# Performance work log

Measured on AMD Instinct MI355X. Metric: run time of the kernel, lower is better.

## Reference

```python
import jax, jax.numpy as jnp
import numpy as np

N, E, G = 50000, 500000, 1024
ND, ED, H, L, OUT = 32, 16, 128, 4, 1
BN_EPS = 1e-5


def setup_inputs() -> dict:
    key = jax.random.key(0)
    ks = jax.random.split(key, 32)

    def w(k, shape, fan):
        return jax.random.normal(k, shape, jnp.float32) / np.float32(np.sqrt(fan))

    inp = {
        "x": jax.random.normal(ks[0], (N, ND), jnp.float32),
        "edge_index": jax.random.randint(ks[1], (2, E), 0, N, jnp.int64),
        "edge_attr": jax.random.normal(ks[2], (E, ED), jnp.float32),
        "batch": jax.random.randint(ks[3], (N,), 0, G, jnp.int64),
        # embeddings
        "ne_w": w(ks[4], (ND, H), ND), "ne_b": jnp.zeros((H,), jnp.float32),
        "ee_w": w(ks[5], (ED, H), ED), "ee_b": jnp.zeros((H,), jnp.float32),
        # per-layer node_mlp: Linear(2H,H) ReLU Linear(H,H) BN(H)
        "nm_w1": w(ks[6], (L, 2 * H, H), 2 * H), "nm_b1": jnp.zeros((L, H), jnp.float32),
        "nm_w2": w(ks[7], (L, H, H), H), "nm_b2": jnp.zeros((L, H), jnp.float32),
        "bn_g": jnp.ones((L, H), jnp.float32), "bn_b": jnp.zeros((L, H), jnp.float32),
        # per-layer edge_mlp: Linear(H,H) ReLU Linear(H,H)  (edge_dim==hidden_dim inside MPNN)
        "em_w1": w(ks[8], (L, H, H), H), "em_b1": jnp.zeros((L, H), jnp.float32),
        "em_w2": w(ks[9], (L, H, H), H), "em_b2": jnp.zeros((L, H), jnp.float32),
        # readout: Linear(H,H) ReLU Dropout(eval=identity) Linear(H,OUT)
        "ro_w1": w(ks[10], (H, H), H), "ro_b1": jnp.zeros((H,), jnp.float32),
        "ro_w2": w(ks[11], (H, OUT), H), "ro_b2": jnp.zeros((OUT,), jnp.float32),
    }
    return inp


def reference(x, edge_index, edge_attr, batch,
              ne_w, ne_b, ee_w, ee_b,
              nm_w1, nm_b1, nm_w2, nm_b2, bn_g, bn_b,
              em_w1, em_b1, em_w2, em_b2,
              ro_w1, ro_b1, ro_w2, ro_b2):
    src, dst = edge_index[0], edge_index[1]  # PyG default: x_j from source, aggregate at target
    h = x @ ne_w + ne_b                      # [N, H]
    e = edge_attr @ ee_w + ee_b              # [E, H]
    inv_std = np.float32(1.0 / np.sqrt(1.0 + BN_EPS))  # eval BN, running_mean=0, running_var=1
    for l in range(nm_w1.shape[0]):
        # edge_mlp
        e = jax.nn.relu(e @ em_w1[l] + em_b1[l]) @ em_w2[l] + em_b2[l]
        # message: concat(x_j, edge_attr) -> node_mlp
        msg = jnp.concatenate([h[src], e], axis=1)              # [E, 2H]
        msg = jax.nn.relu(msg @ nm_w1[l] + nm_b1[l]) @ nm_w2[l] + nm_b2[l]
        msg = msg * (inv_std * bn_g[l]) + bn_b[l]               # BatchNorm1d (eval)
        # scatter-add aggregation + residual update
        agg = jax.ops.segment_sum(msg, dst, num_segments=h.shape[0])
        h = agg + h
    pooled = jax.ops.segment_sum(h, batch, num_segments=G)      # global_add_pool -> [G, H]
    return jax.nn.relu(pooled @ ro_w1 + ro_b1) @ ro_w2 + ro_b2  # [G, OUT]
```

## Files before the change

kernel.cpp:

```cpp
#include <hip/hip_runtime.h>
#include <hip/hip_bf16.h>
#include <math.h>

#define NN 50000
#define EE 500000
#define GG 1024
#define NDIM 32
#define EDIM 16
#define HH 128
#define LL 4
#define TE 64
#define NTE ((EE + TE - 1) / TE)
#define NB2 ((NN + 127) / 128)
#define SCAN_NB ((NN + 255) / 256)

typedef unsigned short ushortT;
typedef __attribute__((ext_vector_type(8))) short bf16x8;
typedef __attribute__((ext_vector_type(4))) float f32x4;

#define MFMA16(a, b, c) __builtin_amdgcn_mfma_f32_16x16x32_bf16(a, b, c, 0, 0, 0)

__device__ inline float bf2f(ushortT u) {
    union { unsigned int i; float f; } v; v.i = ((unsigned int)u) << 16; return v.f;
}
__device__ inline ushortT f2bf(float f) {
    __hip_bfloat16 h = __float2bfloat16(f);
    return *reinterpret_cast<ushortT*>(&h);
}
__device__ inline short f2bfs(float f) { return (short)f2bf(f); }

__device__ inline bf16x8 lds_a(const char* base, int strideB, int row, int colByte,
                               int mask) {
    int b = row * strideB + colByte;
    b ^= ((row & mask) << 4);
    return *reinterpret_cast<const bf16x8*>(base + b);
}

__global__ __launch_bounds__(256) void hist_kernel(
        const int* __restrict__ dst, int* __restrict__ counts) {
    int i = blockIdx.x * 256 + threadIdx.x;
    if (i < EE) atomicAdd(&counts[dst[i]], 1);
}

__global__ __launch_bounds__(256) void scan_part1(
        const int* __restrict__ counts, int* __restrict__ bsum) {
    __shared__ int buf[256];
    int t = threadIdx.x;
    int i = blockIdx.x * 256 + t;
    buf[t] = (i < NN) ? counts[i] : 0;
    __syncthreads();
    for (int s = 128; s > 0; s >>= 1) {
        if (t < s) buf[t] += buf[t + s];
        __syncthreads();
    }
    if (t == 0) bsum[blockIdx.x] = buf[0];
}

__global__ __launch_bounds__(256) void scan_part2(
        const int* __restrict__ bsum, int* __restrict__ bbase) {
    __shared__ int buf[256];
    int t = threadIdx.x;
    int v = (t < SCAN_NB) ? bsum[t] : 0;
    buf[t] = v;
    __syncthreads();
    for (int off = 1; off < 256; off <<= 1) {
        int s = (t >= off) ? buf[t - off] : 0;
        __syncthreads();
        buf[t] += s;
        __syncthreads();
    }
    if (t < SCAN_NB) bbase[t] = buf[t] - v;
}

__global__ __launch_bounds__(256) void scan_part3(
        const int* __restrict__ counts, const int* __restrict__ bbase,
        int* __restrict__ base) {
    __shared__ int buf[256];
    int t = threadIdx.x;
    int i = blockIdx.x * 256 + t;
    int v = (i < NN) ? counts[i] : 0;
    buf[t] = v;
    __syncthreads();
    for (int off = 1; off < 256; off <<= 1) {
        int s = (t >= off) ? buf[t - off] : 0;
        __syncthreads();
        buf[t] += s;
        __syncthreads();
    }
    if (i < NN) base[i] = bbase[blockIdx.x] + buf[t] - v;
}

__global__ __launch_bounds__(256) void build_perm_kernel(
        const int* __restrict__ src, const int* __restrict__ dst,
        const int* __restrict__ base, int* __restrict__ cnt,
        int* __restrict__ perm, int* __restrict__ srcS, int* __restrict__ dstS) {
    int i = blockIdx.x * 256 + threadIdx.x;
    if (i >= EE) return;
    int d = dst[i];
    int pos = base[d] + atomicAdd(&cnt[d], 1);
    perm[pos] = i;
    srcS[pos] = src[i];
    dstS[pos] = d;
}

__global__ __launch_bounds__(256) void ghist_kernel(
        const int* __restrict__ batch, int* __restrict__ gcounts) {
    int i = blockIdx.x * 256 + threadIdx.x;
    if (i < NN) atomicAdd(&gcounts[batch[i]], 1);
}

__global__ __launch_bounds__(1024) void gscan_kernel(
        const int* __restrict__ gcounts, int* __restrict__ gbase) {
    __shared__ int buf[1024];
    int t = threadIdx.x;
    int v = gcounts[t];
    buf[t] = v;
    __syncthreads();
    for (int off = 1; off < 1024; off <<= 1) {
        int s = (t >= off) ? buf[t - off] : 0;
        __syncthreads();
        buf[t] += s;
        __syncthreads();
    }
    gbase[t] = buf[t] - v;
}

__global__ __launch_bounds__(256) void gbuild_kernel(
        const int* __restrict__ batch, const int* __restrict__ gbase,
        int* __restrict__ gcnt, int* __restrict__ gperm) {
    int i = blockIdx.x * 256 + threadIdx.x;
    if (i >= NN) return;
    int b = batch[i];
    int pos = gbase[b] + atomicAdd(&gcnt[b], 1);
    gperm[pos] = i;
}

__global__ __launch_bounds__(256) void transpose_kernel(
        const float* __restrict__ in, ushortT* __restrict__ out, int K, int N) {
    int per = K * N;
    int total = LL * per;
    int idx = blockIdx.x * 256 + threadIdx.x;
    if (idx >= total) return;
    int l = idx / per, rem = idx - l * per;
    int n = rem / K, k = rem - n * K;
    out[idx] = f2bf(in[(size_t)l * per + (size_t)k * N + n]);
}

__global__ __launch_bounds__(256) void transpose_pad32_kernel(
        const float* __restrict__ in, ushortT* __restrict__ out, int KIN) {
    int idx = blockIdx.x * 256 + threadIdx.x;
    if (idx >= HH * 32) return;
    int n = idx >> 5, k = idx & 31;
    out[idx] = (k < KIN) ? f2bf(in[k * HH + n]) : (ushortT)0;
}

__global__ __launch_bounds__(256) void bnfold_kernel(
        const float* __restrict__ w2, const float* __restrict__ b2,
        const float* __restrict__ bng, const float* __restrict__ bnb,
        ushortT* __restrict__ w2g, float* __restrict__ nb2g, float inv_std) {
    int idx = blockIdx.x * 256 + threadIdx.x;
    if (idx < LL * HH * HH) {
        int l = idx / (HH * HH), rem = idx - l * (HH * HH);
        int n = rem / HH, k = rem - n * HH;
        w2g[idx] = f2bf(w2[(size_t)l * HH * HH + (size_t)k * HH + n] *
                        bng[l * HH + n] * inv_std);
    }
    if (idx < LL * HH) {
        nb2g[idx] = b2[idx] * bng[idx] * inv_std + bnb[idx];
    }
}

template<int K, int KS, bool HASB>
__device__ inline void gemm_b(const char* aBase, int aStrideB, int aMask,
        const ushortT* __restrict__ wT, const float* __restrict__ bias,
        int wr, int wc, int l15, int lg, f32x4 acc[2][4]) {
#pragma unroll
    for (int ntl = 0; ntl < 4; ++ntl) {
        float bb = HASB ? bias[wc * 64 + ntl * 16 + l15] : 0.f;
        f32x4 iv = {bb, bb, bb, bb};
        acc[0][ntl] = iv;
        acc[1][ntl] = iv;
    }
#pragma unroll
    for (int ks = 0; ks < K / 32; ++ks) {
        int kk = ks * 32 + lg * 8;
        bf16x8 a0 = lds_a(aBase, aStrideB, wr * 32 + l15,      kk * 2, aMask);
        bf16x8 a1 = lds_a(aBase, aStrideB, wr * 32 + 16 + l15, kk * 2, aMask);
#pragma unroll
        for (int ntl = 0; ntl < 4; ++ntl) {
            int n = wc * 64 + ntl * 16 + l15;
            bf16x8 b = *reinterpret_cast<const bf16x8*>(wT + (size_t)n * KS + kk);
            acc[0][ntl] = MFMA16(a0, b, acc[0][ntl]);
            acc[1][ntl] = MFMA16(a1, b, acc[1][ntl]);
        }
    }
}

__device__ inline void gemm_uinit3(const char* aBase, const char* uBase,
        const ushortT* __restrict__ wT,
        int wr, int wc, int l15, int lg, f32x4 acc[2][4]) {
#pragma unroll
    for (int mt = 0; mt < 2; ++mt)
#pragma unroll
        for (int ntl = 0; ntl < 4; ++ntl) {
            int col = wc * 64 + ntl * 16 + l15;
#pragma unroll
            for (int r = 0; r < 4; ++r) {
                int row = wr * 32 + mt * 16 + lg * 4 + r;
                int b = row * 256 + col * 2; b ^= ((row & 7) << 4);
                acc[mt][ntl][r] = bf2f(*reinterpret_cast<const ushortT*>(uBase + b));
            }
        }
#pragma unroll
    for (int ks = 0; ks < 4; ++ks) {
        int kk = ks * 32 + lg * 8;
        bf16x8 a0 = lds_a(aBase, 256, wr * 32 + l15,      kk * 2, 7);
        bf16x8 a1 = lds_a(aBase, 256, wr * 32 + 16 + l15, kk * 2, 7);
#pragma unroll
        for (int ntl = 0; ntl < 4; ++ntl) {
            int n = wc * 64 + ntl * 16 + l15;
            bf16x8 b = *reinterpret_cast<const bf16x8*>(wT + (size_t)n * 256 + kk);
            acc[0][ntl] = MFMA16(a0, b, acc[0][ntl]);
            acc[1][ntl] = MFMA16(a1, b, acc[1][ntl]);
        }
    }
}

__device__ inline void wfrag(char* base, int wr, int wc, int l15, int lg,
                             f32x4 acc[2][4], bool relu) {
#pragma unroll
    for (int mt = 0; mt < 2; ++mt)
#pragma unroll
        for (int ntl = 0; ntl < 4; ++ntl) {
            int col = wc * 64 + ntl * 16 + l15;
#pragma unroll
            for (int r = 0; r < 4; ++r) {
                int row = wr * 32 + mt * 16 + lg * 4 + r;
                int b = row * 256 + col * 2;
                b ^= ((row & 7) << 4);
                float v = acc[mt][ntl][r];
                if (relu) v = fmaxf(v, 0.f);
                *reinterpret_cast<ushortT*>(base + b) = f2bf(v);
            }
        }
}

template<int EMBED, int LASTL>
__global__ __launch_bounds__(256) void edgeA_kernel(
        const ushortT* __restrict__ u, ushortT* __restrict__ e,
        const int* __restrict__ srcS, const int* __restrict__ dstS,
        const int* __restrict__ basep, const int* __restrict__ perm,
        const float* __restrict__ ea,
        const ushortT* __restrict__ eewT, const float* __restrict__ eeb,
        const ushortT* __restrict__ ew1t, const float* __restrict__ eb1,
        const ushortT* __restrict__ ew2t, const float* __restrict__ eb2,
        const ushortT* __restrict__ nw1bt,
        ushortT* __restrict__ partials) {
    __shared__ __align__(16) char ldsAB[2 * TE * 256];
    __shared__ int dstx[TE], bstartL[TE], sidx[TE], pidx[TE];
    char* eT = ldsAB;
    char* uT = ldsAB + TE * 256;

    const int e0 = blockIdx.x * TE;
    int V = EE - e0; if (V > TE) V = TE;
    const int tid = threadIdx.x;
    const bf16x8 z8 = {0, 0, 0, 0, 0, 0, 0, 0};

    if (tid < TE) {
        int ii = e0 + tid;
        int d = (ii < EE) ? dstS[ii] : -1;
        dstx[tid] = d;
        bstartL[tid] = (d >= 0) ? basep[d] : 0;
        sidx[tid] = (ii < EE) ? srcS[ii] : 0;
        if (EMBED) pidx[tid] = (ii < EE) ? perm[ii] : 0;
    }
    __syncthreads();

#pragma unroll
    for (int s = 0; s < 4; ++s) {
        int idx = tid + s * 256;
        int row = idx >> 4, c8 = (idx & 15) * 8;
        bf16x8 v = *reinterpret_cast<const bf16x8*>(u + (size_t)sidx[row] * HH + c8);
        int b = row * 256 + c8 * 2; b ^= ((row & 7) << 4);
        *reinterpret_cast<bf16x8*>(uT + b) = v;
    }
    if (EMBED) {
        {
            int row = tid >> 2, q4 = (tid & 3) * 4;
            float4 v = *reinterpret_cast<const float4*>(
                ea + (size_t)pidx[row] * EDIM + q4);
            unsigned long long pack =
                (unsigned long long)f2bf(v.x) |
                ((unsigned long long)f2bf(v.y) << 16) |
                ((unsigned long long)f2bf(v.z) << 32) |
                ((unsigned long long)f2bf(v.w) << 48);
            int b = row * 64 + q4 * 2; b ^= ((row & 3) << 4);
            *reinterpret_cast<unsigned long long*>(eT + b) = pack;
        }
        if (tid < 128) {
            int row = tid >> 1;
            int b = row * 64 + 32 + (tid & 1) * 16; b ^= ((row & 3) << 4);
            *reinterpret_cast<bf16x8*>(eT + b) = z8;
        }
    } else {
#pragma unroll
        for (int s = 0; s < 4; ++s) {
            int idx = tid + s * 256;
            int row = idx >> 4, c8 = (idx & 15) * 8;
            bf16x8 v = *reinterpret_cast<const bf16x8*>(
                e + (size_t)(e0 + row) * HH + c8);
            int b = row * 256 + c8 * 2; b ^= ((row & 7) << 4);
            *reinterpret_cast<bf16x8*>(eT + b) = v;
        }
    }
    __syncthreads();

    const int wid = tid >> 6, lane = tid & 63;
    const int wr = wid >> 1, wc = wid & 1, l15 = lane & 15, lg = lane >> 4;
    f32x4 acc[2][4];

    if (EMBED) {
        gemm_b<32, 32, true>(eT, 64, 3, eewT, eeb, wr, wc, l15, lg, acc);
        __syncthreads();
        wfrag(eT, wr, wc, l15, lg, acc, false);
        __syncthreads();
    }
    gemm_b<HH, HH, true>(eT, 256, 7, ew1t, eb1, wr, wc, l15, lg, acc);
    __syncthreads();
    wfrag(eT, wr, wc, l15, lg, acc, true);
    __syncthreads();
    gemm_b<HH, HH, true>(eT, 256, 7, ew2t, eb2, wr, wc, l15, lg, acc);
    __syncthreads();
    wfrag(eT, wr, wc, l15, lg, acc, false);
    __syncthreads();
    if (!LASTL) {
#pragma unroll
        for (int s = 0; s < 4; ++s) {
            int idx = tid + s * 256;
            int row = idx >> 4, c8 = (idx & 15) * 8;
            if (row < V) {
                int b = row * 256 + c8 * 2; b ^= ((row & 7) << 4);
                *reinterpret_cast<bf16x8*>(e + (size_t)(e0 + row) * HH + c8) =
                    *reinterpret_cast<const bf16x8*>(eT + b);
            }
        }
    }
    gemm_uinit3(eT, uT, nw1bt, wr, wc, l15, lg, acc);
    __syncthreads();
    {
#pragma unroll
        for (int mt = 0; mt < 2; ++mt)
#pragma unroll
            for (int ntl = 0; ntl < 4; ++ntl) {
                int col = wc * 64 + ntl * 16 + l15;
#pragma unroll
                for (int r = 0; r < 4; ++r) {
                    int row = wr * 32 + mt * 16 + lg * 4 + r;
                    int b = row * 512 + col * 4;
                    b ^= ((row & 7) << 4);
                    *reinterpret_cast<float*>(ldsAB + b) =
                        fmaxf(acc[mt][ntl][r], 0.f);
                }
            }
    }
    __syncthreads();

    {
        int col = tid & 127, seg = tid >> 7;
        int r = seg * 32, rend = r + 32;
        float sum = 0.f;
        int dprev = -1, runStart = r;
        for (; r < rend; ++r) {
            int d = dstx[r];
            if (d != dprev) {
                if (dprev >= 0) {
                    int slot = ((e0 + runStart) >> 5) - (bstartL[runStart] >> 5);
                    if (slot < 3)
                        partials[((size_t)slot * NN + dprev) * HH + col] = f2bf(sum);
                }
                sum = 0.f; dprev = d; runStart = r;
            }
            if (d >= 0) {
                int b = r * 512 + col * 4; b ^= ((r & 7) << 4);
                sum += *reinterpret_cast<const float*>(ldsAB + b);
            }
        }
        if (dprev >= 0) {
            int slot = ((e0 + runStart) >> 5) - (bstartL[runStart] >> 5);
            if (slot < 3)
                partials[((size_t)slot * NN + dprev) * HH + col] = f2bf(sum);
        }
    }
}

template<int HASU>
__global__ __launch_bounds__(512) void nodeB_kernel(
        const ushortT* __restrict__ partials, const int* __restrict__ basep,
        const ushortT* __restrict__ w2g, const float* __restrict__ nb2g,
        float* __restrict__ h,
        const ushortT* __restrict__ w1tn, const float* __restrict__ b1n,
        ushortT* __restrict__ uOut) {
    __shared__ __align__(16) char sT[128 * 256];
    __shared__ int degx[128];
    __shared__ int basex[128];
    const int n0 = blockIdx.x * 128;
    int V = NN - n0; if (V > 128) V = 128;
    const int tid = threadIdx.x;

    if (tid < 128) {
        int bs = 0, de = 0;
        if (tid < V) {
            int n = n0 + tid;
            bs = basep[n];
            int be = (n + 1 < NN) ? basep[n + 1] : EE;
            de = be - bs;
        }
        basex[tid] = bs;
        degx[tid] = de;
    }
    __syncthreads();

#pragma unroll
    for (int g = 0; g < 4; ++g) {
        int node = g * 32 + (tid >> 4);
        int c8 = (tid & 15) * 8;
        float s[8] = {0.f, 0.f, 0.f, 0.f, 0.f, 0.f, 0.f, 0.f};
        if (node < V) {
            int bs = basex[node], de = degx[node];
            if (de > 0) {
                int ns = ((bs + de - 1) >> 5) - (bs >> 5) + 1;
                if (ns > 3) ns = 3;
                for (int sl = 0; sl < ns; ++sl) {
                    bf16x8 pv = *reinterpret_cast<const bf16x8*>(
                        partials + ((size_t)sl * NN + n0 + node) * HH + c8);
#pragma unroll
                    for (int j = 0; j < 8; ++j) s[j] += bf2f((ushortT)pv[j]);
                }
            }
        }
        bf16x8 o;
#pragma unroll
        for (int j = 0; j < 8; ++j) o[j] = f2bfs(s[j]);
        int b = node * 256 + c8 * 2; b ^= ((node & 7) << 4);
        *reinterpret_cast<bf16x8*>(sT + b) = o;
    }
    __syncthreads();

    const int wid = tid >> 6, lane = tid & 63;
    const int wr = wid >> 1, wc = wid & 1, l15 = lane & 15, lg = lane >> 4;
    f32x4 acc[2][4];

    gemm_b<HH, HH, false>(sT, 256, 7, w2g, nullptr, wr, wc, l15, lg, acc);
#pragma unroll
    for (int ntl = 0; ntl < 4; ++ntl) {
        int col = wc * 64 + ntl * 16 + l15;
        float bg = nb2g[col];
#pragma unroll
        for (int mt = 0; mt < 2; ++mt)
#pragma unroll
            for (int r = 0; r < 4; ++r) {
                int row = wr * 32 + mt * 16 + lg * 4 + r;
                if (row < V) {
                    size_t off = (size_t)(n0 + row) * HH + col;
                    float hn = h[off] + acc[mt][ntl][r] + (float)degx[row] * bg;
                    h[off] = hn;
                    acc[mt][ntl][r] = hn;
                } else {
                    acc[mt][ntl][r] = 0.f;
                }
            }
    }
    if (HASU) {
        __syncthreads();
        wfrag(sT, wr, wc, l15, lg, acc, false);
        __syncthreads();
        gemm_b<HH, 2 * HH, true>(sT, 256, 7, w1tn, b1n, wr, wc, l15, lg, acc);
        __syncthreads();
        wfrag(sT, wr, wc, l15, lg, acc, false);
        __syncthreads();
#pragma unroll
        for (int s = 0; s < 4; ++s) {
            int idx = tid + s * 512;
            int row = idx >> 4, c8 = (idx & 15) * 8;
            if (row < V) {
                int b = row * 256 + c8 * 2; b ^= ((row & 7) << 4);
                *reinterpret_cast<bf16x8*>(uOut + (size_t)(n0 + row) * HH + c8) =
                    *reinterpret_cast<const bf16x8*>(sT + b);
            }
        }
    }
}

__global__ __launch_bounds__(512) void node_pre2_kernel(
        const float* __restrict__ x, const ushortT* __restrict__ newT,
        const float* __restrict__ neb,
        const ushortT* __restrict__ w1t, const float* __restrict__ b1,
        float* __restrict__ h, ushortT* __restrict__ uo) {
    __shared__ __align__(16) char sT[128 * 256];
    __shared__ __align__(16) char xT[128 * 64];
    const int n0 = blockIdx.x * 128;
    int V = NN - n0; if (V > 128) V = 128;
    const int tid = threadIdx.x;

#pragma unroll
    for (int s = 0; s < 2; ++s) {
        int idx = tid + s * 512;
        int row = idx >> 3;
        int q4 = (idx & 7) * 4;
        unsigned long long pack = 0ull;
        if (row < V) {
            float4 v = *reinterpret_cast<const float4*>(
                x + (size_t)(n0 + row) * NDIM + q4);
            pack = (unsigned long long)f2bf(v.x) |
                   ((unsigned long long)f2bf(v.y) << 16) |
                   ((unsigned long long)f2bf(v.z) << 32) |
                   ((unsigned long long)f2bf(v.w) << 48);
        }
        int b = row * 64 + q4 * 2; b ^= ((row & 3) << 4);
        *reinterpret_cast<unsigned long long*>(xT + b) = pack;
    }
    __syncthreads();

    const int wid = tid >> 6, lane = tid & 63;
    const int wr = wid >> 1, wc = wid & 1, l15 = lane & 15, lg = lane >> 4;
    f32x4 acc[2][4];
    gemm_b<32, 32, true>(xT, 64, 3, newT, neb, wr, wc, l15, lg, acc);
#pragma unroll
    for (int mt = 0; mt < 2; ++mt)
#pragma unroll
        for (int ntl = 0; ntl < 4; ++ntl) {
            int col = wc * 64 + ntl * 16 + l15;
#pragma unroll
            for (int r = 0; r < 4; ++r) {
                int row = wr * 32 + mt * 16 + lg * 4 + r;
                if (row < V) h[(size_t)(n0 + row) * HH + col] = acc[mt][ntl][r];
            }
        }
    wfrag(sT, wr, wc, l15, lg, acc, false);
    __syncthreads();
    gemm_b<HH, 2 * HH, true>(sT, 256, 7, w1t, b1, wr, wc, l15, lg, acc);
    __syncthreads();
    wfrag(sT, wr, wc, l15, lg, acc, false);
    __syncthreads();
#pragma unroll
    for (int s = 0; s < 4; ++s) {
        int idx = tid + s * 512;
        int row = idx >> 4, c8 = (idx & 15) * 8;
        if (row < V) {
            int b = row * 256 + c8 * 2; b ^= ((row & 7) << 4);
            *reinterpret_cast<bf16x8*>(uo + (size_t)(n0 + row) * HH + c8) =
                *reinterpret_cast<const bf16x8*>(sT + b);
        }
    }
}

__global__ __launch_bounds__(256) void pool2_kernel(
        const float* __restrict__ h, const int* __restrict__ gperm,
        const int* __restrict__ gbase, const int* __restrict__ gcounts,
        float* __restrict__ pooled) {
    int w = threadIdx.x >> 6, lane = threadIdx.x & 63;
    int g = blockIdx.x * 4 + w;
    int bs = gbase[g], cnt = gcounts[g];
    int c = lane * 2;
    float ax = 0.f, ay = 0.f;
    for (int j = 0; j < cnt; ++j) {
        int n = gperm[bs + j];
        float2 v = *reinterpret_cast<const float2*>(h + (size_t)n * HH + c);
        ax += v.x; ay += v.y;
    }
    float2 o = {ax, ay};
    *reinterpret_cast<float2*>(pooled + (size_t)g * HH + c) = o;
}

__global__ __launch_bounds__(128) void readout_kernel(
        const float* __restrict__ pooled,
        const float* __restrict__ w1, const float* __restrict__ b1,
        const float* __restrict__ w2, const float* __restrict__ b2,
        float* __restrict__ out) {
    __shared__ float row[HH];
    __shared__ float red[HH];
    int g = blockIdx.x, j = threadIdx.x;
    row[j] = pooled[(size_t)g * HH + j];
    __syncthreads();
    float acc = b1[j];
    for (int k = 0; k < HH; ++k) acc += row[k] * w1[k * HH + j];
    red[j] = fmaxf(acc, 0.f) * w2[j];
    __syncthreads();
    for (int s = 64; s > 0; s >>= 1) {
        if (j < s) red[j] += red[j + s];
        __syncthreads();
    }
    if (j == 0) out[g] = red[0] + b2[0];
}

extern "C" void kernel_launch(void* const* d_in, const int* in_sizes, int n_in,
                              void* d_out, int out_size, void* d_ws, size_t ws_size,
                              hipStream_t stream) {
    const float* x     = (const float*)d_in[0];
    const int*   ei    = (const int*)d_in[1];
    const float* ea    = (const float*)d_in[2];
    const int*   batch = (const int*)d_in[3];
    const float* ne_w  = (const float*)d_in[4];
    const float* ne_b  = (const float*)d_in[5];
    const float* ee_w  = (const float*)d_in[6];
    const float* ee_b  = (const float*)d_in[7];
    const float* nm_w1 = (const float*)d_in[8];
    const float* nm_b1 = (const float*)d_in[9];
    const float* nm_w2 = (const float*)d_in[10];
    const float* nm_b2 = (const float*)d_in[11];
    const float* bn_g  = (const float*)d_in[12];
    const float* bn_b  = (const float*)d_in[13];
    const float* em_w1 = (const float*)d_in[14];
    const float* em_b1 = (const float*)d_in[15];
    const float* em_w2 = (const float*)d_in[16];
    const float* em_b2 = (const float*)d_in[17];
    const float* ro_w1 = (const float*)d_in[18];
    const float* ro_b1 = (const float*)d_in[19];
    const float* ro_w2 = (const float*)d_in[20];
    const float* ro_b2 = (const float*)d_in[21];

    const int* srcp = ei;
    const int* dstp = ei + EE;

    char* p = (char*)d_ws;
    float* h = (float*)p;            p += (size_t)NN * HH * 4;
    float* pooled = (float*)p;       p += (size_t)GG * HH * 4;
    ushortT* ebuf = (ushortT*)p;     p += (size_t)EE * HH * 2;
    ushortT* ubuf = (ushortT*)p;     p += (size_t)NN * HH * 2;
    ushortT* partials = (ushortT*)p; p += (size_t)3 * NN * HH * 2;
    ushortT* ew1t = (ushortT*)p;     p += (size_t)LL * HH * HH * 2;
    ushortT* ew2t = (ushortT*)p;     p += (size_t)LL * HH * HH * 2;
    ushortT* nw1t = (ushortT*)p;     p += (size_t)LL * 2 * HH * HH * 2;
    ushortT* w2g  = (ushortT*)p;     p += (size_t)LL * HH * HH * 2;
    float* nb2g   = (float*)p;       p += (size_t)LL * HH * 4;
    ushortT* eewT = (ushortT*)p;     p += (size_t)HH * 32 * 2;
    ushortT* newT = (ushortT*)p;     p += (size_t)HH * 32 * 2;
    int* perm   = (int*)p;           p += (size_t)EE * 4;
    int* srcS   = (int*)p;           p += (size_t)EE * 4;
    int* dstS   = (int*)p;           p += (size_t)EE * 4;
    int* counts = (int*)p;           p += (size_t)NN * 4;
    int* basep  = (int*)p;           p += (size_t)NN * 4;
    int* cnt    = (int*)p;           p += (size_t)NN * 4;
    int* bsum   = (int*)p;           p += (size_t)SCAN_NB * 4;
    int* bbase  = (int*)p;           p += (size_t)SCAN_NB * 4;
    int* gperm  = (int*)p;           p += (size_t)NN * 4;
    int* gcounts= (int*)p;           p += (size_t)GG * 4;
    int* gbase  = (int*)p;           p += (size_t)GG * 4;
    int* gcnt   = (int*)p;           p += (size_t)GG * 4;

    hipMemsetAsync(counts, 0, (size_t)NN * 4, stream);
    hipMemsetAsync(cnt, 0, (size_t)NN * 4, stream);
    hipMemsetAsync(gcounts, 0, (size_t)GG * 4, stream);
    hipMemsetAsync(gcnt, 0, (size_t)GG * 4, stream);
    hist_kernel<<<(EE + 255) / 256, 256, 0, stream>>>(dstp, counts);
    scan_part1<<<SCAN_NB, 256, 0, stream>>>(counts, bsum);
    scan_part2<<<1, 256, 0, stream>>>(bsum, bbase);
    scan_part3<<<SCAN_NB, 256, 0, stream>>>(counts, bbase, basep);
    build_perm_kernel<<<(EE + 255) / 256, 256, 0, stream>>>(
        srcp, dstp, basep, cnt, perm, srcS, dstS);

    ghist_kernel<<<(NN + 255) / 256, 256, 0, stream>>>(batch, gcounts);
    gscan_kernel<<<1, 1024, 0, stream>>>(gcounts, gbase);
    gbuild_kernel<<<(NN + 255) / 256, 256, 0, stream>>>(batch, gbase, gcnt, gperm);

    const float inv_std = 1.0f / sqrtf(1.0f + 1e-5f);
    transpose_kernel<<<(LL * HH * HH + 255) / 256, 256, 0, stream>>>(em_w1, ew1t, HH, HH);
    transpose_kernel<<<(LL * HH * HH + 255) / 256, 256, 0, stream>>>(em_w2, ew2t, HH, HH);
    transpose_kernel<<<(LL * 2 * HH * HH + 255) / 256, 256, 0, stream>>>(nm_w1, nw1t, 2 * HH, HH);
    bnfold_kernel<<<(LL * HH * HH + 255) / 256, 256, 0, stream>>>(
        nm_w2, nm_b2, bn_g, bn_b, w2g, nb2g, inv_std);
    transpose_pad32_kernel<<<(HH * 32 + 255) / 256, 256, 0, stream>>>(ee_w, eewT, EDIM);
    transpose_pad32_kernel<<<(HH * 32 + 255) / 256, 256, 0, stream>>>(ne_w, newT, NDIM);

    node_pre2_kernel<<<NB2, 512, 0, stream>>>(x, newT, ne_b, nw1t, nm_b1, h, ubuf);

    for (int l = 0; l < LL; ++l) {
        const ushortT* nw1bt = nw1t + (size_t)l * 2 * HH * HH + 128;
        if (l == 0) {
            edgeA_kernel<1, 0><<<NTE, 256, 0, stream>>>(
                ubuf, ebuf, srcS, dstS, basep, perm, ea, eewT, ee_b,
                ew1t + (size_t)l * HH * HH, em_b1 + l * HH,
                ew2t + (size_t)l * HH * HH, em_b2 + l * HH,
                nw1bt, partials);
        } else if (l < LL - 1) {
            edgeA_kernel<0, 0><<<NTE, 256, 0, stream>>>(
                ubuf, ebuf, srcS, dstS, basep, perm, ea, eewT, ee_b,
                ew1t + (size_t)l * HH * HH, em_b1 + l * HH,
                ew2t + (size_t)l * HH * HH, em_b2 + l * HH,
                nw1bt, partials);
        } else {
            edgeA_kernel<0, 1><<<NTE, 256, 0, stream>>>(
                ubuf, ebuf, srcS, dstS, basep, perm, ea, eewT, ee_b,
                ew1t + (size_t)l * HH * HH, em_b1 + l * HH,
                ew2t + (size_t)l * HH * HH, em_b2 + l * HH,
                nw1bt, partials);
        }
        if (l < LL - 1) {
            nodeB_kernel<1><<<NB2, 512, 0, stream>>>(
                partials, basep, w2g + (size_t)l * HH * HH, nb2g + l * HH, h,
                nw1t + (size_t)(l + 1) * 2 * HH * HH, nm_b1 + (l + 1) * HH, ubuf);
        } else {
            nodeB_kernel<0><<<NB2, 512, 0, stream>>>(
                partials, basep, w2g + (size_t)l * HH * HH, nb2g + l * HH, h,
                nw1t, nm_b1, ubuf);
        }
    }

    pool2_kernel<<<GG / 4, 256, 0, stream>>>(h, gperm, gbase, gcounts, pooled);
    readout_kernel<<<GG, 128, 0, stream>>>(pooled, ro_w1, ro_b1, ro_w2, ro_b2,
                                           (float*)d_out);
}
```

Measured before the change: 1.230 ms.

## Split fused edge kernel into edge-MLP kernel and gather/message kernel

The fused per-layer edge kernel is split in two. A new edge-MLP kernel uses 128-edge tiles and 512 threads and always writes e back to global memory. A separate gather/message kernel reads u[src] and e, runs the node_mlp first GEMM and the segmented partial reduction. The aim is likely to lower register and LDS pressure and raise occupancy for each phase, at the cost of an extra global write and read of the E×H bf16 edge tensor per layer, including the last layer, which previously skipped the store.

New measurement: 1.315 ms. 7.0% more time.

```diff
diff --git a/kernel.cpp b/kernel.cpp
--- a/kernel.cpp
+++ b/kernel.cpp
@@ -11,6 +11,7 @@
 #define LL 4
 #define TE 64
 #define NTE ((EE + TE - 1) / TE)
+#define ND2 ((EE + 127) / 128)
 #define NB2 ((NN + 127) / 128)
 #define SCAN_NB ((NN + 255) / 256)
 
@@ -245,19 +246,89 @@
         }
 }
 
-template<int EMBED, int LASTL>
-__global__ __launch_bounds__(256) void edgeA_kernel(
-        const ushortT* __restrict__ u, ushortT* __restrict__ e,
-        const int* __restrict__ srcS, const int* __restrict__ dstS,
-        const int* __restrict__ basep, const int* __restrict__ perm,
+template<int EMBED>
+__global__ __launch_bounds__(512) void edgeD_kernel(
+        ushortT* __restrict__ e, const int* __restrict__ perm,
         const float* __restrict__ ea,
         const ushortT* __restrict__ eewT, const float* __restrict__ eeb,
         const ushortT* __restrict__ ew1t, const float* __restrict__ eb1,
-        const ushortT* __restrict__ ew2t, const float* __restrict__ eb2,
+        const ushortT* __restrict__ ew2t, const float* __restrict__ eb2) {
+    __shared__ __align__(16) char eT[128 * 256];
+    const int e0 = blockIdx.x * 128;
+    int V = EE - e0; if (V > 128) V = 128;
+    const int tid = threadIdx.x;
+    const bf16x8 z8 = {0, 0, 0, 0, 0, 0, 0, 0};
+
+    if (EMBED) {
+        int row = tid >> 2, q4 = (tid & 3) * 4;
+        unsigned long long pack = 0ull;
+        if (row < V) {
+            int pp = perm[e0 + row];
+            float4 v = *reinterpret_cast<const float4*>(ea + (size_t)pp * EDIM + q4);
+            pack = (unsigned long long)f2bf(v.x) |
+                   ((unsigned long long)f2bf(v.y) << 16) |
+                   ((unsigned long long)f2bf(v.z) << 32) |
+                   ((unsigned long long)f2bf(v.w) << 48);
+        }
+        int b = row * 64 + q4 * 2; b ^= ((row & 3) << 4);
+        *reinterpret_cast<unsigned long long*>(eT + b) = pack;
+        if (tid < 256) {
+            int prow = tid >> 1;
+            int bb = prow * 64 + 32 + (tid & 1) * 16; bb ^= ((prow & 3) << 4);
+            *reinterpret_cast<bf16x8*>(eT + bb) = z8;
+        }
+    } else {
+#pragma unroll
+        for (int s = 0; s < 4; ++s) {
+            int idx = tid + s * 512;
+            int row = idx >> 4, c8 = (idx & 15) * 8;
+            bf16x8 v = z8;
+            if (row < V)
+                v = *reinterpret_cast<const bf16x8*>(e + (size_t)(e0 + row) * HH + c8);
+            int b = row * 256 + c8 * 2; b ^= ((row & 7) << 4);
+            *reinterpret_cast<bf16x8*>(eT + b) = v;
+        }
+    }
+    __syncthreads();
+
+    const int wid = tid >> 6, lane = tid & 63;
+    const int wr = wid >> 1, wc = wid & 1, l15 = lane & 15, lg = lane >> 4;
+    f32x4 acc[2][4];
+
+    if (EMBED) {
+        gemm_b<32, 32, true>(eT, 64, 3, eewT, eeb, wr, wc, l15, lg, acc);
+        __syncthreads();
+        wfrag(eT, wr, wc, l15, lg, acc, false);
+        __syncthreads();
+    }
+    gemm_b<HH, HH, true>(eT, 256, 7, ew1t, eb1, wr, wc, l15, lg, acc);
+    __syncthreads();
+    wfrag(eT, wr, wc, l15, lg, acc, true);
+    __syncthreads();
+    gemm_b<HH, HH, true>(eT, 256, 7, ew2t, eb2, wr, wc, l15, lg, acc);
+    __syncthreads();
+    wfrag(eT, wr, wc, l15, lg, acc, false);
+    __syncthreads();
+#pragma unroll
+    for (int s = 0; s < 4; ++s) {
+        int idx = tid + s * 512;
+        int row = idx >> 4, c8 = (idx & 15) * 8;
+        if (row < V) {
+            int b = row * 256 + c8 * 2; b ^= ((row & 7) << 4);
+            *reinterpret_cast<bf16x8*>(e + (size_t)(e0 + row) * HH + c8) =
+                *reinterpret_cast<const bf16x8*>(eT + b);
+        }
+    }
+}
+
+__global__ __launch_bounds__(256) void edgeG_kernel(
+        const ushortT* __restrict__ u, const ushortT* __restrict__ e,
+        const int* __restrict__ srcS, const int* __restrict__ dstS,
+        const int* __restrict__ basep,
         const ushortT* __restrict__ nw1bt,
         ushortT* __restrict__ partials) {
     __shared__ __align__(16) char ldsAB[2 * TE * 256];
-    __shared__ int dstx[TE], bstartL[TE], sidx[TE], pidx[TE];
+    __shared__ int dstx[TE], bstartL[TE], sidx[TE];
     char* eT = ldsAB;
     char* uT = ldsAB + TE * 256;
 
@@ -272,7 +343,6 @@
         dstx[tid] = d;
         bstartL[tid] = (d >= 0) ? basep[d] : 0;
         sidx[tid] = (ii < EE) ? srcS[ii] : 0;
-        if (EMBED) pidx[tid] = (ii < EE) ? perm[ii] : 0;
     }
     __syncthreads();
 
@@ -280,38 +350,13 @@
     for (int s = 0; s < 4; ++s) {
         int idx = tid + s * 256;
         int row = idx >> 4, c8 = (idx & 15) * 8;
-        bf16x8 v = *reinterpret_cast<const bf16x8*>(u + (size_t)sidx[row] * HH + c8);
+        bf16x8 uv = *reinterpret_cast<const bf16x8*>(u + (size_t)sidx[row] * HH + c8);
+        bf16x8 ev = z8;
+        if (e0 + row < EE)
+            ev = *reinterpret_cast<const bf16x8*>(e + (size_t)(e0 + row) * HH + c8);
         int b = row * 256 + c8 * 2; b ^= ((row & 7) << 4);
-        *reinterpret_cast<bf16x8*>(uT + b) = v;
-    }
-    if (EMBED) {
-        {
-            int row = tid >> 2, q4 = (tid & 3) * 4;
-            float4 v = *reinterpret_cast<const float4*>(
-                ea + (size_t)pidx[row] * EDIM + q4);
-            unsigned long long pack =
-                (unsigned long long)f2bf(v.x) |
-                ((unsigned long long)f2bf(v.y) << 16) |
-                ((unsigned long long)f2bf(v.z) << 32) |
-                ((unsigned long long)f2bf(v.w) << 48);
-            int b = row * 64 + q4 * 2; b ^= ((row & 3) << 4);
-            *reinterpret_cast<unsigned long long*>(eT + b) = pack;
-        }
-        if (tid < 128) {
-            int row = tid >> 1;
-            int b = row * 64 + 32 + (tid & 1) * 16; b ^= ((row & 3) << 4);
-            *reinterpret_cast<bf16x8*>(eT + b) = z8;
-        }
-    } else {
-#pragma unroll
-        for (int s = 0; s < 4; ++s) {
-            int idx = tid + s * 256;
-            int row = idx >> 4, c8 = (idx & 15) * 8;
-            bf16x8 v = *reinterpret_cast<const bf16x8*>(
-                e + (size_t)(e0 + row) * HH + c8);
-            int b = row * 256 + c8 * 2; b ^= ((row & 7) << 4);
-            *reinterpret_cast<bf16x8*>(eT + b) = v;
-        }
+        *reinterpret_cast<bf16x8*>(uT + b) = uv;
+        *reinterpret_cast<bf16x8*>(eT + b) = ev;
     }
     __syncthreads();
 
@@ -319,50 +364,21 @@
     const int wr = wid >> 1, wc = wid & 1, l15 = lane & 15, lg = lane >> 4;
     f32x4 acc[2][4];
 
-    if (EMBED) {
-        gemm_b<32, 32, true>(eT, 64, 3, eewT, eeb, wr, wc, l15, lg, acc);
-        __syncthreads();
-        wfrag(eT, wr, wc, l15, lg, acc, false);
-        __syncthreads();
-    }
-    gemm_b<HH, HH, true>(eT, 256, 7, ew1t, eb1, wr, wc, l15, lg, acc);
-    __syncthreads();
-    wfrag(eT, wr, wc, l15, lg, acc, true);
-    __syncthreads();
-    gemm_b<HH, HH, true>(eT, 256, 7, ew2t, eb2, wr, wc, l15, lg, acc);
-    __syncthreads();
-    wfrag(eT, wr, wc, l15, lg, acc, false);
-    __syncthreads();
-    if (!LASTL) {
-#pragma unroll
-        for (int s = 0; s < 4; ++s) {
-            int idx = tid + s * 256;
-            int row = idx >> 4, c8 = (idx & 15) * 8;
-            if (row < V) {
-                int b = row * 256 + c8 * 2; b ^= ((row & 7) << 4);
-                *reinterpret_cast<bf16x8*>(e + (size_t)(e0 + row) * HH + c8) =
-                    *reinterpret_cast<const bf16x8*>(eT + b);
-            }
-        }
-    }
     gemm_uinit3(eT, uT, nw1bt, wr, wc, l15, lg, acc);
     __syncthreads();
-    {
-#pragma unroll
-        for (int mt = 0; mt < 2; ++mt)
-#pragma unroll
-            for (int ntl = 0; ntl < 4; ++ntl) {
-                int col = wc * 64 + ntl * 16 + l15;
-#pragma unroll
-                for (int r = 0; r < 4; ++r) {
-                    int row = wr * 32 + mt * 16 + lg * 4 + r;
-                    int b = row * 512 + col * 4;
-                    b ^= ((row & 7) << 4);
-                    *reinterpret_cast<float*>(ldsAB + b) =
-                        fmaxf(acc[mt][ntl][r], 0.f);
-                }
-            }
-    }
+#pragma unroll
+    for (int mt = 0; mt < 2; ++mt)
+#pragma unroll
+        for (int ntl = 0; ntl < 4; ++ntl) {
+            int col = wc * 64 + ntl * 16 + l15;
+#pragma unroll
+            for (int r = 0; r < 4; ++r) {
+                int row = wr * 32 + mt * 16 + lg * 4 + r;
+                int b = row * 512 + col * 4;
+                b ^= ((row & 7) << 4);
+                *reinterpret_cast<float*>(ldsAB + b) = fmaxf(acc[mt][ntl][r], 0.f);
+            }
+        }
     __syncthreads();
 
     {
@@ -677,24 +693,18 @@
     for (int l = 0; l < LL; ++l) {
         const ushortT* nw1bt = nw1t + (size_t)l * 2 * HH * HH + 128;
         if (l == 0) {
-            edgeA_kernel<1, 0><<<NTE, 256, 0, stream>>>(
-                ubuf, ebuf, srcS, dstS, basep, perm, ea, eewT, ee_b,
+            edgeD_kernel<1><<<ND2, 512, 0, stream>>>(
+                ebuf, perm, ea, eewT, ee_b,
                 ew1t + (size_t)l * HH * HH, em_b1 + l * HH,
-                ew2t + (size_t)l * HH * HH, em_b2 + l * HH,
-                nw1bt, partials);
-        } else if (l < LL - 1) {
-            edgeA_kernel<0, 0><<<NTE, 256, 0, stream>>>(
-                ubuf, ebuf, srcS, dstS, basep, perm, ea, eewT, ee_b,
+                ew2t + (size_t)l * HH * HH, em_b2 + l * HH);
+        } else {
+            edgeD_kernel<0><<<ND2, 512, 0, stream>>>(
+                ebuf, perm, ea, eewT, ee_b,
                 ew1t + (size_t)l * HH * HH, em_b1 + l * HH,
-                ew2t + (size_t)l * HH * HH, em_b2 + l * HH,
-                nw1bt, partials);
-        } else {
-            edgeA_kernel<0, 1><<<NTE, 256, 0, stream>>>(
-                ubuf, ebuf, srcS, dstS, basep, perm, ea, eewT, ee_b,
-                ew1t + (size_t)l * HH * HH, em_b1 + l * HH,
-                ew2t + (size_t)l * HH * HH, em_b2 + l * HH,
-                nw1bt, partials);
-        }
+                ew2t + (size_t)l * HH * HH, em_b2 + l * HH);
+        }
+        edgeG_kernel<<<NTE, 256, 0, stream>>>(
+            ubuf, ebuf, srcS, dstS, basep, nw1bt, partials);
         if (l < LL - 1) {
             nodeB_kernel<1><<<NB2, 512, 0, stream>>>(
                 partials, basep, w2g + (size_t)l * HH * HH, nb2g + l * HH, h,
```
